# Performance work log

Measured on AMD Instinct MI355X. Metric: run time of the kernel, lower is better.

## Reference

```python
import jax, jax.numpy as jnp
import numpy as np
import math

B, L, D, K, G = 4, 4096, 2048, 4, 8  # batch, seq_len, d_model, kernel_size, num_group


def setup_inputs() -> dict:
    key = jax.random.key(0)
    k1, k2 = jax.random.split(key)
    x = jax.random.normal(k1, (B, L, D), dtype=jnp.float32)
    # torch Conv1d weight is [O=D, I=D//G, K]; kaiming-uniform-ish scale.
    fan_in = (D // G) * K
    w = jax.random.normal(k2, (K, D // G, D), dtype=jnp.float32) * (1.0 / math.sqrt(fan_in))
    return {"x": x, "w": w}


def reference(x, w):
    # x: [B, L, D] (module transposes to NCL internally; we stay channels-last).
    # torch pads both sides by K-1 then slices off the trailing K-1 outputs,
    # which is exactly a left-only (causal) pad of K-1.
    k = w.shape[0]
    groups = x.shape[-1] // w.shape[1]
    out = jax.lax.conv_general_dilated(
        x, w,
        window_strides=(1,),
        padding=[(k - 1, 0)],
        dimension_numbers=("NHC", "HIO", "NHC"),
        feature_group_count=groups,
    )
    return out  # [B, L, D]
```

## Files before the change

kernel.cpp:

```cpp
#include <hip/hip_runtime.h>
#include <stdint.h>


#define CC_L 4096
#define CC_D 2048

typedef float f32x4 __attribute__((ext_vector_type(4)));
typedef __bf16 bf16x8 __attribute__((ext_vector_type(8)));

static __device__ __forceinline__ unsigned short f2bf(float f) {
    union { float f; uint32_t u; } v; v.f = f;
    uint32_t u = v.u;
    u += 0x7fffu + ((u >> 16) & 1u);
    return (unsigned short)(u >> 16);
}

static __device__ __forceinline__ void glds16(const void* g, void* l) {
    __builtin_amdgcn_global_load_lds(
        (const __attribute__((address_space(1))) uint32_t*)g,
        (__attribute__((address_space(3))) uint32_t*)l, 16, 0, 0);
}

__global__ __launch_bounds__(256) void cc_prep_w(const float* __restrict__ w,
                                                 unsigned short* __restrict__ wt) {
    __shared__ unsigned short T[64][136];
    const int tid = threadIdx.x;
    const int k  = blockIdx.x >> 6;
    const int ot = (blockIdx.x >> 1) & 31;
    const int ih = blockIdx.x & 1;
    const int o0 = ot << 6;
    const int i0 = ih << 7;

#pragma unroll
    for (int it = 0; it < 8; ++it) {
        int i  = it * 16 + (tid >> 4);
        int oc = (tid & 15) << 2;
        const float4 v = *(const float4*)(w + ((size_t)(k * 256 + i0 + i)) * CC_D + o0 + oc);
        T[oc + 0][i] = f2bf(v.x);
        T[oc + 1][i] = f2bf(v.y);
        T[oc + 2][i] = f2bf(v.z);
        T[oc + 3][i] = f2bf(v.w);
    }
    __syncthreads();
#pragma unroll
    for (int it = 0; it < 4; ++it) {
        int o  = it * 16 + (tid >> 4);
        int ic = (tid & 15) << 3;
        *(uint4*)(wt + (size_t)(o0 + o) * 1024 + k * 256 + i0 + ic) = *(const uint4*)&T[o][ic];
    }
}

__global__ __launch_bounds__(256, 3) void cc_conv(const float* __restrict__ x,
                                                  const unsigned short* __restrict__ wt,
                                                  float* __restrict__ out) {
    __shared__ unsigned short As[131][72];
    __shared__ unsigned short Bs[2][128][64];

    const int tid   = threadIdx.x;
    const int tileN = blockIdx.x & 15;
    const int tileM = blockIdx.x >> 4;
    const int n0    = tileN << 7;
    const int g     = tileN >> 1;
    const int cin   = g << 8;
    const int m0    = tileM << 7;
    const int b     = m0 >> 12;
    const int l0    = m0 & (CC_L - 1);

    const int lane = tid & 63;
    const int wv   = tid >> 6;
    const int wm   = (wv & 1) << 6;
    const int wn   = (wv >> 1) << 6;
    const int lr   = lane & 15;
    const int quad = lane >> 4;

    const int b_row = lane >> 3;
    const int b_q   = (lane & 7) ^ b_row;

    const float* xg = x + (size_t)b * CC_L * CC_D + cin;

    f32x4 acc[4][4];
#pragma unroll
    for (int i = 0; i < 4; ++i)
#pragma unroll
        for (int j = 0; j < 4; ++j) acc[i][j] = (f32x4){0.f, 0.f, 0.f, 0.f};

    const int f4 = tid & 15;
    const int rb = tid >> 4;
    float4 avm[8];
    float4 avh;

#define LOAD_A(cc)                                                                  \
    {                                                                               \
        _Pragma("unroll")                                                           \
        for (int j = 0; j < 8; ++j) {                                               \
            int l = l0 + rb + j * 16;                                               \
            avm[j] = *(const float4*)(xg + (size_t)l * CC_D + ((cc) << 6) + (f4 << 2)); \
        }                                                                           \
        if (tid < 48) {                                                             \
            int l = l0 - 3 + (tid >> 4);                                            \
            avh = *(const float4*)(xg + (size_t)(l < 0 ? 0 : l) * CC_D + ((cc) << 6) + (f4 << 2)); \
        }                                                                           \
    }

#define WRITE_A()                                                                   \
    {                                                                               \
        _Pragma("unroll")                                                           \
        for (int j = 0; j < 8; ++j) {                                               \
            ushort4 h;                                                              \
            h.x = f2bf(avm[j].x); h.y = f2bf(avm[j].y);                             \
            h.z = f2bf(avm[j].z); h.w = f2bf(avm[j].w);                             \
            *(ushort4*)&As[rb + j * 16 + 3][f4 << 2] = h;                           \
        }                                                                           \
        if (tid < 48) {                                                             \
            ushort4 h = {0, 0, 0, 0};                                               \
            if (l0 > 0) {                                                           \
                h.x = f2bf(avh.x); h.y = f2bf(avh.y);                               \
                h.z = f2bf(avh.z); h.w = f2bf(avh.w);                               \
            }                                                                       \
            *(ushort4*)&As[tid >> 4][f4 << 2] = h;                                  \
        }                                                                           \
    }

#define ISSUE_B(buf, stp)                                                           \
    {                                                                               \
        const unsigned short* gb = wt + (size_t)n0 * 1024 + (((stp) & 3) << 8)      \
                                   + (((stp) >> 2) << 6);                           \
        _Pragma("unroll")                                                           \
        for (int it = 0; it < 4; ++it) {                                            \
            int rowbase = (wv << 5) + (it << 3);                                    \
            glds16(gb + (size_t)(rowbase + b_row) * 1024 + (b_q << 3),              \
                   &Bs[buf][rowbase][0]);                                           \
        }                                                                           \
    }

    LOAD_A(0);
    ISSUE_B(0, 0);
    WRITE_A();
    LOAD_A(1);
    __syncthreads();

    for (int s = 0; s < 16; ++s) {
        if (s < 15) ISSUE_B((s + 1) & 1, s + 1);
        const int kf = s & 3;
        const int pb = s & 1;
#pragma unroll
        for (int ks = 0; ks < 2; ++ks) {
            bf16x8 a[4], bb[4];
#pragma unroll
            for (int f = 0; f < 4; ++f)
                a[f] = *(const bf16x8*)&As[wm + f * 16 + lr + kf][(ks << 5) + (quad << 3)];
#pragma unroll
            for (int f = 0; f < 4; ++f) {
                int n    = wn + f * 16 + lr;
                int slot = ((ks << 2) + quad) ^ (lr & 7);
                bb[f] = *(const bf16x8*)&Bs[pb][n][slot << 3];
            }
#pragma unroll
            for (int fm = 0; fm < 4; ++fm)
#pragma unroll
                for (int fn = 0; fn < 4; ++fn)
                    acc[fm][fn] = __builtin_amdgcn_mfma_f32_16x16x32_bf16(
                        a[fm], bb[fn], acc[fm][fn], 0, 0, 0);
        }
        if (kf == 3 && s < 15) {
            __syncthreads();
            WRITE_A();
            int ccn = (s >> 2) + 2;
            if (ccn < 4) LOAD_A(ccn);
        }
        if (s < 15) __syncthreads();
    }

    const size_t obase = (size_t)m0 * CC_D + n0;
#pragma unroll
    for (int fm = 0; fm < 4; ++fm)
#pragma unroll
        for (int fn = 0; fn < 4; ++fn) {
            int ml = wm + fm * 16 + quad * 4;
            int nl = wn + fn * 16 + lr;
#pragma unroll
            for (int r = 0; r < 4; ++r)
                out[obase + (size_t)(ml + r) * CC_D + nl] = acc[fm][fn][r];
        }
}

extern "C" void kernel_launch(void* const* d_in, const int* in_sizes, int n_in,
                              void* d_out, int out_size, void* d_ws, size_t ws_size,
                              hipStream_t stream) {
    const float* x = (const float*)d_in[0];
    const float* w = (const float*)d_in[1];
    float* out = (float*)d_out;
    unsigned short* wt = (unsigned short*)d_ws;

    cc_prep_w<<<256, 256, 0, stream>>>(w, wt);
    cc_conv<<<2048, 256, 0, stream>>>(x, wt, out);
}
```

Measured before the change: 268.2 us.

## Load weight fragments directly from global memory and double-buffer A tiles

Drops the LDS staging of the weight tile (global_load_lds into Bs). Each lane now reads its bf16 weight fragments straight from global memory/L2, and the freed LDS is used to double-buffer the activation tile, so the loop needs one barrier per 64-channel chunk instead of two per step. Block indices are remapped so each XCD handles a fixed pair of N tiles, which is meant to keep weight reuse inside that XCD's L2. The prep kernel now transposes in fp32 and converts after the transpose. The risk is higher global-load latency and redundant weight reads by the two M-waves, which could stall the MFMAs.

```diff
diff --git a/kernel.cpp b/kernel.cpp
--- a/kernel.cpp
+++ b/kernel.cpp
@@ -15,15 +15,9 @@
     return (unsigned short)(u >> 16);
 }
 
-static __device__ __forceinline__ void glds16(const void* g, void* l) {
-    __builtin_amdgcn_global_load_lds(
-        (const __attribute__((address_space(1))) uint32_t*)g,
-        (__attribute__((address_space(3))) uint32_t*)l, 16, 0, 0);
-}
-
 __global__ __launch_bounds__(256) void cc_prep_w(const float* __restrict__ w,
                                                  unsigned short* __restrict__ wt) {
-    __shared__ unsigned short T[64][136];
+    __shared__ float T[64][129];
     const int tid = threadIdx.x;
     const int k  = blockIdx.x >> 6;
     const int ot = (blockIdx.x >> 1) & 31;
@@ -36,29 +30,38 @@
         int i  = it * 16 + (tid >> 4);
         int oc = (tid & 15) << 2;
         const float4 v = *(const float4*)(w + ((size_t)(k * 256 + i0 + i)) * CC_D + o0 + oc);
-        T[oc + 0][i] = f2bf(v.x);
-        T[oc + 1][i] = f2bf(v.y);
-        T[oc + 2][i] = f2bf(v.z);
-        T[oc + 3][i] = f2bf(v.w);
+        T[oc + 0][i] = v.x;
+        T[oc + 1][i] = v.y;
+        T[oc + 2][i] = v.z;
+        T[oc + 3][i] = v.w;
     }
     __syncthreads();
 #pragma unroll
     for (int it = 0; it < 4; ++it) {
         int o  = it * 16 + (tid >> 4);
         int ic = (tid & 15) << 3;
-        *(uint4*)(wt + (size_t)(o0 + o) * 1024 + k * 256 + i0 + ic) = *(const uint4*)&T[o][ic];
+        ushort4 h0, h1;
+        h0.x = f2bf(T[o][ic + 0]); h0.y = f2bf(T[o][ic + 1]);
+        h0.z = f2bf(T[o][ic + 2]); h0.w = f2bf(T[o][ic + 3]);
+        h1.x = f2bf(T[o][ic + 4]); h1.y = f2bf(T[o][ic + 5]);
+        h1.z = f2bf(T[o][ic + 6]); h1.w = f2bf(T[o][ic + 7]);
+        unsigned short* dst = wt + (size_t)(o0 + o) * 1024 + k * 256 + i0 + ic;
+        *(ushort4*)(dst + 0) = h0;
+        *(ushort4*)(dst + 4) = h1;
     }
 }
 
 __global__ __launch_bounds__(256, 3) void cc_conv(const float* __restrict__ x,
                                                   const unsigned short* __restrict__ wt,
                                                   float* __restrict__ out) {
-    __shared__ unsigned short As[131][72];
-    __shared__ unsigned short Bs[2][128][64];
+    __shared__ unsigned short As[2][131][72];
 
     const int tid   = threadIdx.x;
-    const int tileN = blockIdx.x & 15;
-    const int tileM = blockIdx.x >> 4;
+    const int bid   = blockIdx.x;
+    const int xcd   = bid & 7;
+    const int jj    = bid >> 3;
+    const int tileN = (xcd << 1) | (jj >> 7);
+    const int tileM = jj & 127;
     const int n0    = tileN << 7;
     const int g     = tileN >> 1;
     const int cin   = g << 8;
@@ -73,10 +76,8 @@
     const int lr   = lane & 15;
     const int quad = lane >> 4;
 
-    const int b_row = lane >> 3;
-    const int b_q   = (lane & 7) ^ b_row;
-
     const float* xg = x + (size_t)b * CC_L * CC_D + cin;
+    const unsigned short* wp = wt + (size_t)(n0 + wn + lr) * 1024 + (quad << 3);
 
     f32x4 acc[4][4];
 #pragma unroll
@@ -102,14 +103,14 @@
         }                                                                           \
     }
 
-#define WRITE_A()                                                                   \
+#define WRITE_A(dbuf)                                                               \
     {                                                                               \
         _Pragma("unroll")                                                           \
         for (int j = 0; j < 8; ++j) {                                               \
             ushort4 h;                                                              \
             h.x = f2bf(avm[j].x); h.y = f2bf(avm[j].y);                             \
             h.z = f2bf(avm[j].z); h.w = f2bf(avm[j].w);                             \
-            *(ushort4*)&As[rb + j * 16 + 3][f4 << 2] = h;                           \
+            *(ushort4*)&As[dbuf][rb + j * 16 + 3][f4 << 2] = h;                     \
         }                                                                           \
         if (tid < 48) {                                                             \
             ushort4 h = {0, 0, 0, 0};                                               \
@@ -117,58 +118,46 @@
                 h.x = f2bf(avh.x); h.y = f2bf(avh.y);                               \
                 h.z = f2bf(avh.z); h.w = f2bf(avh.w);                               \
             }                                                                       \
-            *(ushort4*)&As[tid >> 4][f4 << 2] = h;                                  \
-        }                                                                           \
-    }
-
-#define ISSUE_B(buf, stp)                                                           \
-    {                                                                               \
-        const unsigned short* gb = wt + (size_t)n0 * 1024 + (((stp) & 3) << 8)      \
-                                   + (((stp) >> 2) << 6);                           \
-        _Pragma("unroll")                                                           \
-        for (int it = 0; it < 4; ++it) {                                            \
-            int rowbase = (wv << 5) + (it << 3);                                    \
-            glds16(gb + (size_t)(rowbase + b_row) * 1024 + (b_q << 3),              \
-                   &Bs[buf][rowbase][0]);                                           \
+            *(ushort4*)&As[dbuf][tid >> 4][f4 << 2] = h;                            \
         }                                                                           \
     }
 
     LOAD_A(0);
-    ISSUE_B(0, 0);
-    WRITE_A();
-    LOAD_A(1);
+    WRITE_A(0);
     __syncthreads();
 
-    for (int s = 0; s < 16; ++s) {
-        if (s < 15) ISSUE_B((s + 1) & 1, s + 1);
-        const int kf = s & 3;
-        const int pb = s & 1;
 #pragma unroll
-        for (int ks = 0; ks < 2; ++ks) {
-            bf16x8 a[4], bb[4];
+    for (int cc = 0; cc < 4; ++cc) {
+        const int buf = cc & 1;
+        if (cc < 3) LOAD_A(cc + 1);
 #pragma unroll
-            for (int f = 0; f < 4; ++f)
-                a[f] = *(const bf16x8*)&As[wm + f * 16 + lr + kf][(ks << 5) + (quad << 3)];
+        for (int kf = 0; kf < 4; ++kf) {
+            bf16x8 a[2][4], bb[2][4];
 #pragma unroll
-            for (int f = 0; f < 4; ++f) {
-                int n    = wn + f * 16 + lr;
-                int slot = ((ks << 2) + quad) ^ (lr & 7);
-                bb[f] = *(const bf16x8*)&Bs[pb][n][slot << 3];
-            }
+            for (int ks = 0; ks < 2; ++ks)
 #pragma unroll
-            for (int fm = 0; fm < 4; ++fm)
+                for (int f = 0; f < 4; ++f)
+                    bb[ks][f] = *(const bf16x8*)(wp + (size_t)f * 16384
+                                                 + kf * 256 + cc * 64 + ks * 32);
 #pragma unroll
-                for (int fn = 0; fn < 4; ++fn)
-                    acc[fm][fn] = __builtin_amdgcn_mfma_f32_16x16x32_bf16(
-                        a[fm], bb[fn], acc[fm][fn], 0, 0, 0);
+            for (int ks = 0; ks < 2; ++ks)
+#pragma unroll
+                for (int f = 0; f < 4; ++f)
+                    a[ks][f] = *(const bf16x8*)&As[buf][wm + f * 16 + lr + kf]
+                                                  [(ks << 5) + (quad << 3)];
+#pragma unroll
+            for (int ks = 0; ks < 2; ++ks)
+#pragma unroll
+                for (int fm = 0; fm < 4; ++fm)
+#pragma unroll
+                    for (int fn = 0; fn < 4; ++fn)
+                        acc[fm][fn] = __builtin_amdgcn_mfma_f32_16x16x32_bf16(
+                            a[ks][fm], bb[ks][fn], acc[fm][fn], 0, 0, 0);
         }
-        if (kf == 3 && s < 15) {
+        if (cc < 3) {
+            WRITE_A(buf ^ 1);
             __syncthreads();
-            WRITE_A();
-            int ccn = (s >> 2) + 2;
-            if (ccn < 4) LOAD_A(ccn);
         }
-        if (s < 15) __syncthreads();
     }
 
     const size_t obase = (size_t)m0 * CC_D + n0;
```

Result: slower. 366.9 us (+36.8%).
